# Kernel optimization log

Measured on AMD Instinct MI355X. Metric: run time of the kernel, lower is better.

Reference implementation:

```python
import jax, jax.numpy as jnp
import numpy as np

B, S, H = 2, 4096, 1024
NH, BS, NR = 16, 64, 3
HD = H // NH
NB = S // BS
PEN = -10000.0


def setup_inputs():
    key = jax.random.key(0)
    k0, k1, k2, k3 = jax.random.split(key, 4)
    s = 0.02
    inp = {
        'hidden_states': jax.random.normal(k0, (B, S, H), jnp.float32),
        'attention_mask': jnp.ones((B, S), jnp.float32),
        'Wq': jax.random.normal(k1, (H, H), jnp.float32) * s,
        'Wk': jax.random.normal(k2, (H, H), jnp.float32) * s,
        'Wv': jax.random.normal(k3, (H, H), jnp.float32) * s,
        'bq': jnp.zeros((H,), jnp.float32),
        'bk': jnp.zeros((H,), jnp.float32),
        'bv': jnp.zeros((H,), jnp.float32),
    }
    rng = np.random.default_rng(0)
    inp['rand_attn'] = jnp.asarray(rng.integers(1, NB - 1, size=(B, NH, NB - 2, NR)), jnp.int32)
    return inp


def _attend(q_blk, kmat, vmat, mask, rsd):
    # q_blk:[b,h,q,d]  kmat/vmat:[b,h,k,d]  mask: multiplicative {0,1} broadcastable to [b,h,q,k]
    p = jnp.einsum('bhqd,bhkd->bhqk', q_blk, kmat) * rsd + (1.0 - mask) * PEN
    return jnp.einsum('bhqk,bhkd->bhqd', jax.nn.softmax(p, axis=-1), vmat)


def reference(hidden_states, attention_mask, Wq, bq, Wk, bk, Wv, bv, rand_attn):
    b, s, _ = hidden_states.shape
    h, d, bs = NH, HD, BS
    nb = s // bs
    rsd = 1.0 / jnp.sqrt(jnp.asarray(d, hidden_states.dtype))

    def proj(W, bias):
        return (hidden_states @ W + bias).reshape(b, s, h, d).transpose(0, 2, 1, 3)

    q, k, v = proj(Wq, bq), proj(Wk, bk), proj(Wv, bv)  # [b,h,s,d]

    # --- masks (create_masks_for_block_sparse_attn)
    bm = attention_mask.reshape(b, nb, bs)
    band_mask = jnp.einsum('blq,blk->blqk', bm[:, 2:-2],
                           jnp.concatenate([bm[:, 1:-3], bm[:, 2:-2], bm[:, 3:-1]], axis=2))[:, None]
    from_mask = attention_mask.reshape(b, 1, s, 1)
    to_mask = attention_mask.reshape(b, 1, 1, s)

    qb = q.reshape(b, h, nb, bs, d)
    kb = k.reshape(b, h, nb, bs, d)
    vb = v.reshape(b, h, nb, bs, d)

    # --- gather random blocks (jax_gather with batch_dims=2)
    gather2 = jax.vmap(jax.vmap(lambda m, i: m[i]))
    gk = gather2(kb, rand_attn).reshape(b, h, nb - 2, NR * bs, d)
    gv = gather2(vb, rand_attn).reshape(b, h, nb - 2, NR * bs, d)
    rm = jax.vmap(lambda m, i: m[i])(bm, rand_attn).reshape(b, h, nb - 2, NR * bs)
    rand_mask = jnp.einsum('blq,bhlk->bhlqk', bm[:, 1:-1], rm)  # [b,h,nb-2,bs,NR*bs]

    # --- block 0: attends to everything
    first_ctx = _attend(qb[:, :, 0], k, v, to_mask, rsd)[:, :, None]

    # --- block 1: first 3 blocks + last block + its random blocks
    ones_r = jnp.ones((b, 1, 1, NR * bs), q.dtype)
    sk = jnp.concatenate([kb[:, :, 0], kb[:, :, 1], kb[:, :, 2], kb[:, :, -1], gk[:, :, 0]], axis=2)
    sv = jnp.concatenate([vb[:, :, 0], vb[:, :, 1], vb[:, :, 2], vb[:, :, -1], gv[:, :, 0]], axis=2)
    seq_pad = jnp.concatenate([to_mask[:, :, :, :3 * bs], to_mask[:, :, :, -bs:], ones_r], axis=3)
    rand_pad = jnp.concatenate([jnp.ones((b, h, bs, 4 * bs), q.dtype), rand_mask[:, :, 0]], axis=3)
    second_ctx = _attend(qb[:, :, 1], sk, sv, jnp.minimum(seq_pad, rand_pad), rsd)[:, :, None]

    # --- middle blocks 2..nb-3: sliding band + random + first-global + last-global
    mq = qb[:, :, 2:-2]  # [b,h,L,bs,d], L = nb-4
    ek = jnp.concatenate([kb[:, :, 1:-3], kb[:, :, 2:-2], kb[:, :, 3:-1]], axis=3)  # [b,h,L,3bs,d]
    ev = jnp.concatenate([vb[:, :, 1:-3], vb[:, :, 2:-2], vb[:, :, 3:-1]], axis=3)
    band_p = jnp.einsum('bhlqd,bhlkd->bhlqk', mq, ek) * rsd + (1.0 - band_mask) * PEN
    rand_p = jnp.einsum('bhlqd,bhlkd->bhlqk', mq, gk[:, :, 1:-1]) * rsd + (1.0 - rand_mask[:, :, 1:-1]) * PEN
    first_p = jnp.einsum('bhlqd,bhkd->bhlqk', mq, kb[:, :, 0]) * rsd \
        + (1.0 - to_mask[:, :, :, :bs][:, :, :, None]) * PEN
    last_p = jnp.einsum('bhlqd,bhkd->bhlqk', mq, kb[:, :, -1]) * rsd \
        + (1.0 - to_mask[:, :, :, -bs:][:, :, :, None]) * PEN
    # scores layout: [first(bs) | band(3bs) | rand(NR*bs) | last(bs)]
    w = jax.nn.softmax(jnp.concatenate([first_p, band_p, rand_p, last_p], axis=-1), axis=-1)
    mid_ctx = jnp.einsum('bhlqk,bhlkd->bhlqd', w[..., bs:4 * bs], ev)
    mid_ctx += jnp.einsum('bhlqk,bhlkd->bhlqd', w[..., 4 * bs:-bs], gv[:, :, 1:-1])
    mid_ctx += jnp.einsum('bhlqk,bhkd->bhlqd', w[..., :bs], vb[:, :, 0])
    mid_ctx += jnp.einsum('bhlqk,bhkd->bhlqd', w[..., -bs:], vb[:, :, -1])

    # --- block nb-2: first block + last 3 blocks + its random blocks
    slk = jnp.concatenate([kb[:, :, 0], kb[:, :, -3], kb[:, :, -2], kb[:, :, -1], gk[:, :, -1]], axis=2)
    slv = jnp.concatenate([vb[:, :, 0], vb[:, :, -3], vb[:, :, -2], vb[:, :, -1], gv[:, :, -1]], axis=2)
    seq_pad = jnp.concatenate([to_mask[:, :, :, :bs], to_mask[:, :, :, -3 * bs:], ones_r], axis=3)
    rand_pad = jnp.concatenate([jnp.ones((b, h, bs, 4 * bs), q.dtype), rand_mask[:, :, -1]], axis=3)
    seclast_ctx = _attend(qb[:, :, -2], slk, slv, jnp.minimum(seq_pad, rand_pad), rsd)[:, :, None]

    # --- last block: attends to everything
    last_ctx = _attend(qb[:, :, -1], k, v, to_mask, rsd)[:, :, None]

    ctx = jnp.concatenate([first_ctx, second_ctx, mid_ctx, seclast_ctx, last_ctx], axis=2)
    ctx = ctx.reshape(b, h, s, d) * from_mask
    return ctx.transpose(0, 2, 1, 3).reshape(b, s, h * d)
```

## Files before the change

### kernel.cpp

```cpp
#include <hip/hip_runtime.h>

typedef unsigned short u16;
typedef short short8 __attribute__((ext_vector_type(8)));
typedef float f32x4 __attribute__((ext_vector_type(4)));

#define S_TOT 4096
#define NHEAD 16
#define HD 64
#define NB 64
#define BS 64
#define M0 16.0f

__device__ __forceinline__ u16 f2bf(float f) {
    unsigned int u = __builtin_bit_cast(unsigned int, f);
    unsigned int r = (u + 0x7fffu + ((u >> 16) & 1u)) >> 16;
    return (u16)r;
}

__device__ __forceinline__ void gload_lds16(const void* g, void* l) {
    __builtin_amdgcn_global_load_lds(
        (const __attribute__((address_space(1))) unsigned int*)g,
        (__attribute__((address_space(3))) unsigned int*)l, 16, 0, 0);
}

__device__ __forceinline__ float rsum16(float v) {
    v += __shfl_xor(v, 1);
    v += __shfl_xor(v, 2);
    v += __shfl_xor(v, 4);
    v += __shfl_xor(v, 8);
    return v;
}

__global__ __launch_bounds__(256) void convH(const float* __restrict__ h, u16* __restrict__ A) {
    size_t i = (size_t)blockIdx.x * blockDim.x + threadIdx.x;
    float4 v = ((const float4*)h)[i];
    ushort4 o;
    o.x = f2bf(v.x); o.y = f2bf(v.y); o.z = f2bf(v.z); o.w = f2bf(v.w);
    ((ushort4*)A)[i] = o;
}

__global__ __launch_bounds__(256) void transW(const float* __restrict__ Wq,
                                              const float* __restrict__ Wk,
                                              const float* __restrict__ Wv,
                                              u16* __restrict__ Wt) {
    const float* W = blockIdx.z == 0 ? Wq : (blockIdx.z == 1 ? Wk : Wv);
    u16* T = Wt + (size_t)blockIdx.z * 1024 * 1024;
    __shared__ float tile[64][65];
    int n0 = blockIdx.x * 64, k0 = blockIdx.y * 64;
    int tx = threadIdx.x, ty = threadIdx.y;
    for (int r = ty; r < 64; r += 4) tile[r][tx] = W[(size_t)(k0 + r) * 1024 + n0 + tx];
    __syncthreads();
    for (int r = ty; r < 64; r += 4) T[(size_t)(n0 + r) * 1024 + k0 + tx] = f2bf(tile[tx][r]);
}

__global__ __launch_bounds__(256, 2) void gemm_fused(const u16* __restrict__ Ah, const u16* __restrict__ Wt,
                                                     const float* __restrict__ bq, const float* __restrict__ bk,
                                                     const float* __restrict__ bv,
                                                     u16* __restrict__ Qb, u16* __restrict__ Kb,
                                                     u16* __restrict__ Vtb) {
    __shared__ alignas(16) char lds[2][32768];

    int bid = blockIdx.x;
    int xcd = bid & 7, idx = bid >> 3;
    int bm = xcd * 8 + (idx & 7);
    int bn = idx >> 3;
    int m0 = bm * 128, n0 = bn * 128;
    int mode = bn >> 3;
    const float* bias = mode == 0 ? bq : (mode == 1 ? bk : bv);
    int tid = threadIdx.x, wave = tid >> 6, lane = tid & 63;
    int lo = lane & 15, hi = lane >> 4;
    int wr = wave >> 1, wc = wave & 1;

    const char* Ac = (const char*)Ah;
    const char* Wc = (const char*)Wt;

    auto STAGE = [&](int buf, int t) {
#pragma unroll
        for (int i = 0; i < 4; i++) {
            int off = i * 4096 + tid * 16;
            int row = off >> 7, cb = off & 127;
            int cs = cb ^ ((row & 7) << 4);
            char* d = lds[buf] + i * 4096 + wave * 1024;
            gload_lds16(Ac + (size_t)(m0 + row) * 2048 + t * 128 + cs, d);
            gload_lds16(Wc + (size_t)(n0 + row) * 2048 + t * 128 + cs, d + 16384);
        }
    };

    f32x4 acc[4][4];
#pragma unroll
    for (int i = 0; i < 4; i++)
#pragma unroll
        for (int j = 0; j < 4; j++) acc[i][j] = f32x4{0.f, 0.f, 0.f, 0.f};

    STAGE(0, 0);
    asm volatile("s_waitcnt vmcnt(0)" ::: "memory");
    __builtin_amdgcn_s_barrier();
    __builtin_amdgcn_sched_barrier(0);

    for (int t = 0; t < 16; t++) {
        int buf = t & 1;
        if (t < 15) STAGE(buf ^ 1, t + 1);
        const char* As = lds[buf];
        const char* Bs = lds[buf] + 16384;
        short8 b[4][2];
#pragma unroll
        for (int ni = 0; ni < 4; ni++) {
            int row = wc * 64 + ni * 16 + lo;
            int sw = (row & 7) << 4;
#pragma unroll
            for (int kk = 0; kk < 2; kk++)
                b[ni][kk] = *(const short8*)(Bs + row * 128 + ((kk * 64 + hi * 16) ^ sw));
        }
        __builtin_amdgcn_s_setprio(1);
#pragma unroll
        for (int mi = 0; mi < 4; mi++) {
            int row = wr * 64 + mi * 16 + lo;
            int sw = (row & 7) << 4;
            short8 a0 = *(const short8*)(As + row * 128 + ((hi * 16) ^ sw));
            short8 a1 = *(const short8*)(As + row * 128 + ((64 + hi * 16) ^ sw));
#pragma unroll
            for (int ni = 0; ni < 4; ni++) {
                acc[mi][ni] = __builtin_amdgcn_mfma_f32_16x16x32_bf16(a0, b[ni][0], acc[mi][ni], 0, 0, 0);
                acc[mi][ni] = __builtin_amdgcn_mfma_f32_16x16x32_bf16(a1, b[ni][1], acc[mi][ni], 0, 0, 0);
            }
        }
        __builtin_amdgcn_s_setprio(0);
        asm volatile("s_waitcnt vmcnt(0)" ::: "memory");
        __builtin_amdgcn_s_barrier();
        __builtin_amdgcn_sched_barrier(0);
    }

    char* Cs = lds[0];
    int nb0 = n0 & 1023;
    float bv4[4];
#pragma unroll
    for (int ni = 0; ni < 4; ni++) bv4[ni] = bias[nb0 + wc * 64 + ni * 16 + lo];

    if (mode < 2) {
#pragma unroll
        for (int mi = 0; mi < 4; mi++)
#pragma unroll
            for (int ni = 0; ni < 4; ni++)
#pragma unroll
                for (int r = 0; r < 4; r++) {
                    int row = wr * 64 + mi * 16 + hi * 4 + r;
                    int nl = wc * 64 + ni * 16 + lo;
                    *(u16*)(Cs + ((row * 256 + nl * 2) ^ ((row & 7) << 4))) = f2bf(acc[mi][ni][r] + bv4[ni]);
                }
        __syncthreads();
        u16* T = (mode == 0) ? Qb : Kb;
#pragma unroll
        for (int it = 0; it < 8; it++) {
            int off = it * 4096 + tid * 16;
            int row = off >> 8, c = off & 255;
            short8 v = *(const short8*)(Cs + ((row * 256 + c) ^ ((row & 7) << 4)));
            int nm = nb0 + (c >> 1);
            int hh = nm >> 6, d = nm & 63;
            int s = m0 + row;
            int b_ = s >> 12, sr = s & 4095;
            *(short8*)&T[(((size_t)b_ * NHEAD + hh) * S_TOT + sr) * HD + d] = v;
        }
    } else {
#pragma unroll
        for (int mi = 0; mi < 4; mi++)
#pragma unroll
            for (int ni = 0; ni < 4; ni++)
#pragma unroll
                for (int r = 0; r < 4; r++) {
                    int row = wc * 64 + ni * 16 + lo;
                    int ml = wr * 64 + mi * 16 + hi * 4 + r;
                    *(u16*)(Cs + ((row * 256 + ml * 2) ^ ((row & 7) << 4))) = f2bf(acc[mi][ni][r] + bv4[ni]);
                }
        __syncthreads();
#pragma unroll
        for (int it = 0; it < 8; it++) {
            int off = it * 4096 + tid * 16;
            int row = off >> 8, c = off & 255;
            short8 v = *(const short8*)(Cs + ((row * 256 + c) ^ ((row & 7) << 4)));
            int dr = nb0 + row;
            int hh = dr >> 6, d = dr & 63;
            int s = m0 + (c >> 1);
            int b_ = s >> 12, sr = s & 4095;
            *(short8*)&Vtb[(((size_t)b_ * NHEAD + hh) * HD + d) * S_TOT + sr] = v;
        }
    }
}

__global__ __launch_bounds__(256) void bigbird_attn(const u16* __restrict__ Qb, const u16* __restrict__ Kb,
                                                    const u16* __restrict__ Vtb, const float* __restrict__ am,
                                                    const int* __restrict__ rand_attn, float* __restrict__ out,
                                                    float* __restrict__ po, float* __restrict__ pl) {
    int lx = blockIdx.x;
    int h = blockIdx.y, b = blockIdx.z;
    bool heavy = lx < 16;
    int p = lx & 7;
    int l = heavy ? ((lx >> 3) ? 63 : 0) : (lx - 15);
    int bh = b * NHEAD + h;
    const u16* Qh = Qb + (size_t)bh * S_TOT * HD;
    const u16* Kh = Kb + (size_t)bh * S_TOT * HD;
    const u16* Vh = Vtb + (size_t)bh * HD * S_TOT;
    int tid = threadIdx.x, wave = tid >> 6, lane = tid & 63;
    int lo = lane & 15, hi = lane >> 4;

    __shared__ int klist[64];
    __shared__ int knum_s;
    __shared__ alignas(16) u16 Kls[2][64 * 64];
    __shared__ alignas(16) u16 Vls[2][64 * 64];
    __shared__ alignas(16) u16 Plds[4][16 * 64];

    auto STAGE = [&](int buf, int kblk) {
        const char* Kc = (const char*)(Kh + (size_t)kblk * BS * HD);
        const char* Vc = (const char*)(Vh + kblk * BS);
#pragma unroll
        for (int i = 0; i < 2; i++) {
            int off = i * 4096 + wave * 1024 + lane * 16;
            int row = off >> 7, c = off & 127;
            int cs = c ^ ((row & 7) << 4);
            gload_lds16(Kc + row * 128 + cs, (char*)Kls[buf] + i * 4096 + wave * 1024);
            gload_lds16(Vc + row * 8192 + cs, (char*)Vls[buf] + i * 4096 + wave * 1024);
        }
    };

    if (tid == 0) {
        if (heavy) {
            for (int i = 0; i < 8; i++) klist[i] = p * 8 + i;
            knum_s = 8;
        } else {
            int q = 0;
            klist[q++] = 0;
            if (l == 1) { klist[q++] = 1; klist[q++] = 2; }
            else if (l == 62) { klist[q++] = 61; klist[q++] = 62; }
            else { klist[q++] = l - 1; klist[q++] = l; klist[q++] = l + 1; }
            klist[q++] = 63;
            const int* ra = rand_attn + (((size_t)b * NHEAD + h) * 62 + (l - 1)) * 3;
            klist[q++] = ra[0]; klist[q++] = ra[1]; klist[q++] = ra[2];
            knum_s = q;
        }
    }
    STAGE(0, heavy ? p * 8 : 0);
    __syncthreads();

    int kn = knum_s;
    int qrow = l * BS + wave * 16;

    short8 qf[2];
#pragma unroll
    for (int kk = 0; kk < 2; kk++)
        qf[kk] = *(const short8*)&Qh[(size_t)(qrow + lo) * HD + kk * 32 + hi * 8];

    float ls[4];
    f32x4 oacc[4];
#pragma unroll
    for (int r = 0; r < 4; r++) ls[r] = 0.f;
#pragma unroll
    for (int n = 0; n < 4; n++) oacc[n] = f32x4{0.f, 0.f, 0.f, 0.f};
    char* pbase = (char*)&Plds[wave][0];

    int buf = 0;
    for (int ci = 0; ci < kn; ci++) {
        int kbase = klist[ci] * BS;
        if (ci + 1 < kn) STAGE(buf ^ 1, klist[ci + 1]);
        float pen[4];
#pragma unroll
        for (int t = 0; t < 4; t++) pen[t] = (1.0f - am[b * S_TOT + kbase + t * 16 + lo]) * (-10000.0f) - M0;
        f32x4 sc[4];
#pragma unroll
        for (int t = 0; t < 4; t++) {
            f32x4 c = f32x4{0.f, 0.f, 0.f, 0.f};
#pragma unroll
            for (int kk = 0; kk < 2; kk++) {
                int kr = t * 16 + lo;
                int a = (kr * 128 + kk * 64 + hi * 16) ^ ((kr & 7) << 4);
                short8 kf = *(const short8*)((char*)Kls[buf] + a);
                c = __builtin_amdgcn_mfma_f32_16x16x32_bf16(qf[kk], kf, c, 0, 0, 0);
            }
            sc[t] = c;
        }
#pragma unroll
        for (int t = 0; t < 4; t++)
#pragma unroll
            for (int r = 0; r < 4; r++) {
                float pr = __expf(sc[t][r] * 0.125f + pen[t]);
                ls[r] += pr;
                int row = hi * 4 + r, col = t * 16 + lo;
                int off = (row * 128 + col * 2) ^ ((row & 7) << 4);
                *(u16*)(pbase + off) = f2bf(pr);
            }
#pragma unroll
        for (int kk = 0; kk < 2; kk++) {
            int off = (lo * 128 + kk * 64 + hi * 16) ^ ((lo & 7) << 4);
            short8 pf = *(const short8*)(pbase + off);
#pragma unroll
            for (int n = 0; n < 4; n++) {
                int vr = n * 16 + lo;
                int a = (vr * 128 + kk * 64 + hi * 16) ^ ((vr & 7) << 4);
                short8 vf = *(const short8*)((char*)Vls[buf] + a);
                oacc[n] = __builtin_amdgcn_mfma_f32_16x16x32_bf16(pf, vf, oacc[n], 0, 0, 0);
            }
        }
        __syncthreads();
        buf ^= 1;
    }

    if (heavy) {
        int combo = (bh << 1) | (l ? 1 : 0);
        int base = (combo * 8 + p) * 64;
#pragma unroll
        for (int r = 0; r < 4; r++) {
            int qr = wave * 16 + hi * 4 + r;
            float lsum = rsum16(ls[r]);
            if (lo == 0) pl[base + qr] = lsum;
#pragma unroll
            for (int n = 0; n < 4; n++)
                po[(size_t)(base + qr) * 64 + n * 16 + lo] = oacc[n][r];
        }
    } else {
#pragma unroll
        for (int r = 0; r < 4; r++) {
            float lsum = rsum16(ls[r]);
            int q = qrow + hi * 4 + r;
            float qm = am[b * S_TOT + q];
            float iv = qm / lsum;
#pragma unroll
            for (int n = 0; n < 4; n++)
                out[((size_t)b * S_TOT + q) * 1024 + h * HD + n * 16 + lo] = oacc[n][r] * iv;
        }
    }
}

__global__ __launch_bounds__(256) void reduce_heavy(const float* __restrict__ po, const float* __restrict__ pl,
                                                    const float* __restrict__ am, float* __restrict__ out) {
    int combo = blockIdx.x;
    int b = combo >> 5, h = (combo >> 1) & 15, hv = combo & 1;
    int l = hv ? 63 : 0;
    for (int idx = threadIdx.x; idx < 4096; idx += 256) {
        int qr = idx >> 6, d = idx & 63;
        float s = 0.f, lsum = 0.f;
#pragma unroll
        for (int p = 0; p < 8; p++) {
            s += po[(size_t)((combo * 8 + p) * 64 + qr) * 64 + d];
            lsum += pl[(combo * 8 + p) * 64 + qr];
        }
        int q = l * BS + qr;
        float qm = am[b * S_TOT + q];
        out[((size_t)b * S_TOT + q) * 1024 + h * HD + d] = s / lsum * qm;
    }
}

extern "C" void kernel_launch(void* const* d_in, const int* in_sizes, int n_in,
                              void* d_out, int out_size, void* d_ws, size_t ws_size,
                              hipStream_t stream) {
    const float* hidden = (const float*)d_in[0];
    const float* am = (const float*)d_in[1];
    const float* Wq = (const float*)d_in[2];
    const float* Wk = (const float*)d_in[3];
    const float* Wv = (const float*)d_in[4];
    const float* bq = (const float*)d_in[5];
    const float* bk = (const float*)d_in[6];
    const float* bv = (const float*)d_in[7];
    const int* rand_attn = (const int*)d_in[8];
    float* out = (float*)d_out;

    char* w = (char*)d_ws;
    u16* Ah = (u16*)w;  w += (size_t)8192 * 1024 * 2;
    u16* Wt = (u16*)w;  w += (size_t)3 * 1024 * 1024 * 2;
    u16* Qb = (u16*)w;  w += (size_t)2 * 16 * 4096 * 64 * 2;
    u16* Kb = (u16*)w;  w += (size_t)2 * 16 * 4096 * 64 * 2;
    u16* Vtb = (u16*)w;
    float* po = (float*)Ah;
    float* pl = po + (size_t)64 * 8 * 64 * 64;

    convH<<<8192, 256, 0, stream>>>(hidden, Ah);
    transW<<<dim3(16, 16, 3), dim3(64, 4), 0, stream>>>(Wq, Wk, Wv, Wt);
    gemm_fused<<<1536, 256, 0, stream>>>(Ah, Wt, bq, bk, bv, Qb, Kb, Vtb);
    bigbird_attn<<<dim3(78, 16, 2), 256, 0, stream>>>(Qb, Kb, Vtb, am, rand_attn, out, po, pl);
    reduce_heavy<<<64, 256, 0, stream>>>(po, pl, am, out);
}
```

Baseline: 145.1 us.

## Prefetch K two blocks ahead with split waitcnt and remap grid by XCD

Splits K and V staging so K is triple-buffered and prefetched two blocks ahead while V stays double-buffered one ahead. The full __syncthreads is replaced by a partial vmcnt wait plus a raw barrier, so later loads can stay in flight. It also flattens the grid and maps each head's blocks onto the same XCD so that head's K/V can be reused in the shared L2. This costs extra LDS and relies on hand-counted vmcnt, which is fragile if the load counts change.

```diff
diff --git a/kernel.cpp b/kernel.cpp
--- a/kernel.cpp
+++ b/kernel.cpp
@@ -190,12 +190,14 @@
                                                     const u16* __restrict__ Vtb, const float* __restrict__ am,
                                                     const int* __restrict__ rand_attn, float* __restrict__ out,
                                                     float* __restrict__ po, float* __restrict__ pl) {
-    int lx = blockIdx.x;
-    int h = blockIdx.y, b = blockIdx.z;
+    int pid = blockIdx.x;
+    int xcd = pid & 7, slot = pid >> 3;
+    int bh = xcd * 4 + slot / 78;
+    int lx = slot % 78;
+    int b = bh >> 4, h = bh & 15;
     bool heavy = lx < 16;
     int p = lx & 7;
     int l = heavy ? ((lx >> 3) ? 63 : 0) : (lx - 15);
-    int bh = b * NHEAD + h;
     const u16* Qh = Qb + (size_t)bh * S_TOT * HD;
     const u16* Kh = Kb + (size_t)bh * S_TOT * HD;
     const u16* Vh = Vtb + (size_t)bh * HD * S_TOT;
@@ -204,20 +206,26 @@
 
     __shared__ int klist[64];
     __shared__ int knum_s;
-    __shared__ alignas(16) u16 Kls[2][64 * 64];
+    __shared__ alignas(16) u16 Kls[3][64 * 64];
     __shared__ alignas(16) u16 Vls[2][64 * 64];
     __shared__ alignas(16) u16 Plds[4][16 * 64];
 
-    auto STAGE = [&](int buf, int kblk) {
+    auto SK = [&](int s_, int kblk) {
         const char* Kc = (const char*)(Kh + (size_t)kblk * BS * HD);
-        const char* Vc = (const char*)(Vh + kblk * BS);
 #pragma unroll
         for (int i = 0; i < 2; i++) {
             int off = i * 4096 + wave * 1024 + lane * 16;
             int row = off >> 7, c = off & 127;
-            int cs = c ^ ((row & 7) << 4);
-            gload_lds16(Kc + row * 128 + cs, (char*)Kls[buf] + i * 4096 + wave * 1024);
-            gload_lds16(Vc + row * 8192 + cs, (char*)Vls[buf] + i * 4096 + wave * 1024);
+            gload_lds16(Kc + row * 128 + (c ^ ((row & 7) << 4)), (char*)Kls[s_] + i * 4096 + wave * 1024);
+        }
+    };
+    auto SV = [&](int s_, int kblk) {
+        const char* Vc = (const char*)(Vh + kblk * BS);
+#pragma unroll
+        for (int i = 0; i < 2; i++) {
+            int off = i * 4096 + wave * 1024 + lane * 16;
+            int row = off >> 7, c = off & 127;
+            gload_lds16(Vc + (size_t)row * 8192 + (c ^ ((row & 7) << 4)), (char*)Vls[s_] + i * 4096 + wave * 1024);
         }
     };
 
@@ -237,11 +245,13 @@
             knum_s = q;
         }
     }
-    STAGE(0, heavy ? p * 8 : 0);
+    int c0 = heavy ? p * 8 : 0;
+    SK(0, c0);
+    SV(0, c0);
     __syncthreads();
-
     int kn = knum_s;
     int qrow = l * BS + wave * 16;
+    if (1 < kn) SK(1, klist[1]);
 
     short8 qf[2];
 #pragma unroll
@@ -256,10 +266,12 @@
     for (int n = 0; n < 4; n++) oacc[n] = f32x4{0.f, 0.f, 0.f, 0.f};
     char* pbase = (char*)&Plds[wave][0];
 
-    int buf = 0;
     for (int ci = 0; ci < kn; ci++) {
         int kbase = klist[ci] * BS;
-        if (ci + 1 < kn) STAGE(buf ^ 1, klist[ci + 1]);
+        if (ci + 1 < kn) SV((ci + 1) & 1, klist[ci + 1]);
+        if (ci + 2 < kn) SK((ci + 2) % 3, klist[ci + 2]);
+        const char* Kc = (const char*)Kls[ci % 3];
+        const char* Vc = (const char*)Vls[ci & 1];
         float pen[4];
 #pragma unroll
         for (int t = 0; t < 4; t++) pen[t] = (1.0f - am[b * S_TOT + kbase + t * 16 + lo]) * (-10000.0f) - M0;
@@ -271,7 +283,7 @@
             for (int kk = 0; kk < 2; kk++) {
                 int kr = t * 16 + lo;
                 int a = (kr * 128 + kk * 64 + hi * 16) ^ ((kr & 7) << 4);
-                short8 kf = *(const short8*)((char*)Kls[buf] + a);
+                short8 kf = *(const short8*)(Kc + a);
                 c = __builtin_amdgcn_mfma_f32_16x16x32_bf16(qf[kk], kf, c, 0, 0, 0);
             }
             sc[t] = c;
@@ -294,12 +306,19 @@
             for (int n = 0; n < 4; n++) {
                 int vr = n * 16 + lo;
                 int a = (vr * 128 + kk * 64 + hi * 16) ^ ((vr & 7) << 4);
-                short8 vf = *(const short8*)((char*)Vls[buf] + a);
+                short8 vf = *(const short8*)(Vc + a);
                 oacc[n] = __builtin_amdgcn_mfma_f32_16x16x32_bf16(pf, vf, oacc[n], 0, 0, 0);
             }
         }
-        __syncthreads();
-        buf ^= 1;
+        if (ci + 1 < kn) {
+            if (ci + 2 < kn) {
+                asm volatile("s_waitcnt vmcnt(2)" ::: "memory");
+            } else {
+                asm volatile("s_waitcnt vmcnt(0)" ::: "memory");
+            }
+            __builtin_amdgcn_s_barrier();
+            __builtin_amdgcn_sched_barrier(0);
+        }
     }
 
     if (heavy) {
@@ -373,6 +392,6 @@
     convH<<<8192, 256, 0, stream>>>(hidden, Ah);
     transW<<<dim3(16, 16, 3), dim3(64, 4), 0, stream>>>(Wq, Wk, Wv, Wt);
     gemm_fused<<<1536, 256, 0, stream>>>(Ah, Wt, bq, bk, bv, Qb, Kb, Vtb);
-    bigbird_attn<<<dim3(78, 16, 2), 256, 0, stream>>>(Qb, Kb, Vtb, am, rand_attn, out, po, pl);
+    bigbird_attn<<<2496, 256, 0, stream>>>(Qb, Kb, Vtb, am, rand_attn, out, po, pl);
     reduce_heavy<<<64, 256, 0, stream>>>(po, pl, am, out);
 }
```

After: 140.1 us. -3.5%, faster.
